# Performance work log

Hardware: AMD Instinct MI355X
Metric: run time of the kernel (lower is better)

Reference implementation:

```python
import jax, jax.numpy as jnp
import numpy as np

FS = 11      # filter_size per spatial dim
N_ITER = 5   # mean-field iterations


def _gaussian_kernel1d(inv_theta, spacing, fs):
    # distances scaled by per-sample spacing; center tap zeroed (message passing excludes self)
    d = spacing * jnp.arange(-(fs // 2), fs // 2 + 1, dtype=jnp.float32)
    k = jnp.exp(-(d * inv_theta) ** 2 / 2)
    return k * (1.0 - jax.nn.one_hot(fs // 2, fs, dtype=k.dtype))


def _conv1d_last(x, kernel):
    # valid cross-correlation along the last axis; kernel is symmetric so conv == corr
    xr = x.reshape(-1, 1, x.shape[-1])
    out = jax.lax.conv_general_dilated(xr, kernel.reshape(1, 1, -1), (1,), 'VALID')
    return out.reshape(*x.shape[:-1], out.shape[-1])


def _smooth_single(x, spacing, inv_theta):
    # x: (C, H, W) -> separable zero-center Gaussian filter, per-sample kernels
    p = FS // 2
    x = jnp.pad(x, ((0, 0), (p, p), (p, p)))
    kh = _gaussian_kernel1d(inv_theta[0], spacing[0], FS)
    kw = _gaussian_kernel1d(inv_theta[1], spacing[1], FS)
    x = _conv1d_last(jnp.swapaxes(x, 1, 2), kh)  # conv along H -> (C, W+2p, H)
    x = _conv1d_last(jnp.swapaxes(x, 1, 2), kw)  # conv along W -> (C, H, W)
    return x


def setup_inputs() -> dict:
    key = jax.random.key(0)
    k1, = jax.random.split(key, 1)
    x = jax.random.normal(k1, (8, 19, 512, 512), dtype=jnp.float32)
    spatial_spacings = jnp.ones((8, 2), dtype=jnp.float32)
    smoothness_weight = jnp.array(1.0, dtype=jnp.float32)
    inv_smoothness_theta = jnp.ones((2,), dtype=jnp.float32)  # 1 / smoothness_theta
    return {"x": x, "spatial_spacings": spatial_spacings,
            "smoothness_weight": smoothness_weight,
            "inv_smoothness_theta": inv_smoothness_theta}


def reference(x, spatial_spacings, smoothness_weight, inv_smoothness_theta):
    n_classes = x.shape[1]
    comp = -jnp.eye(n_classes, dtype=x.dtype)  # compatibility matrix -(l1 == l2)
    negative_unary = x
    smooth = jax.vmap(_smooth_single, in_axes=(0, 0, None))
    for _ in range(N_ITER):
        q = jax.nn.softmax(x, axis=1)
        m = smoothness_weight * smooth(q, spatial_spacings, inv_smoothness_theta)
        m = jnp.einsum('bchw,cd->bdhw', m, comp)
        x = negative_unary - m
    return x  # returns='logits'
```

## Files before the change

### kernel.cpp

```cpp
#include <hip/hip_runtime.h>

#define FS 11
#define HFS 5

constexpr int Bn = 8, Cn = 19, Hn = 512, Wn = 512;
constexpr int HWn = Hn * Wn;
constexpr int CHWn = Cn * HWn;
constexpr int TOTn = Bn * CHWn;

constexpr int TH = 32, TW = 64;
constexpr int HR  = TH + 10;
constexpr int HC4 = 20;
constexpr int NP4 = HR * HC4;
constexpr int QS  = 84;
constexpr int WSS = 68;

__global__ void k_taps(const float* __restrict__ spacing,
                       const float* __restrict__ inv_theta,
                       const float* __restrict__ wgt,
                       float* __restrict__ taps) {
    int t = threadIdx.x;
    if (t < Bn * 2 * FS) {
        int j = t % FS;
        int dim = (t / FS) & 1;
        int b = t / (2 * FS);
        float d = spacing[b * 2 + dim] * (float)(j - HFS);
        float a = d * inv_theta[dim];
        float k = __expf(-0.5f * a * a);
        if (j == HFS) k = 0.0f;
        if (dim == 1) k *= wgt[0];
        taps[t] = k;
    }
}

__global__ __launch_bounds__(256, 4) void k_fused(const float* __restrict__ xin,
                                                  const float* __restrict__ x0,
                                                  float* __restrict__ xout,
                                                  const float* __restrict__ taps) {
    __shared__ float srinv[HR * QS];
    __shared__ float qs[HR * QS];
    __shared__ float ws[HR * WSS];

    const int tid = threadIdx.x;
    const int w0 = blockIdx.x * TW;
    const int h0 = blockIdx.y * TH;
    const int b  = blockIdx.z;

    const float* tp = taps + b * (2 * FS);
    float kh[FS], kw[FS];
#pragma unroll
    for (int j = 0; j < FS; j++) { kh[j] = tp[j]; kw[j] = tp[FS + j]; }

    const float* xb = xin + b * CHWn;

#pragma unroll 1
    for (int k = 0; k < 4; ++k) {
        int i = tid + 256 * k;
        if (i >= NP4) break;
        int r  = i / HC4, c4 = i % HC4;
        int hh = h0 - 5 + r;
        int ww = w0 - 8 + 4 * c4;
        if (hh >= 0 && hh < Hn && ww >= 0 && ww <= Wn - 4) {
            const float* p = xb + hh * Wn + ww;
            float4 s = {0.f, 0.f, 0.f, 0.f};
#pragma unroll
            for (int c = 0; c < Cn; ++c) {
                float4 v = *(const float4*)(p + c * HWn);
                s.x += __expf(v.x); s.y += __expf(v.y);
                s.z += __expf(v.z); s.w += __expf(v.w);
            }
            float4 rv = {1.f / s.x, 1.f / s.y, 1.f / s.z, 1.f / s.w};
            *(float4*)&srinv[r * QS + 4 * c4] = rv;
        }
    }
    __syncthreads();

    for (int c = 0; c < Cn; ++c) {
        const float* xc = xb + c * HWn;

#pragma unroll 1
        for (int k = 0; k < 4; ++k) {
            int i = tid + 256 * k;
            if (i >= NP4) break;
            int r  = i / HC4, c4 = i % HC4;
            int hh = h0 - 5 + r;
            int ww = w0 - 8 + 4 * c4;
            float4 qv = {0.f, 0.f, 0.f, 0.f};
            if (hh >= 0 && hh < Hn && ww >= 0 && ww <= Wn - 4) {
                float4 v  = *(const float4*)(xc + hh * Wn + ww);
                float4 rv = *(const float4*)&srinv[r * QS + 4 * c4];
                qv.x = __expf(v.x) * rv.x; qv.y = __expf(v.y) * rv.y;
                qv.z = __expf(v.z) * rv.z; qv.w = __expf(v.w) * rv.w;
            }
            *(float4*)&qs[r * QS + 4 * c4] = qv;
        }
        __syncthreads();

#pragma unroll 1
        for (int i = tid; i < HR * 8; i += 256) {
            int r = i >> 3, g = i & 7;
            float t[24];
#pragma unroll
            for (int m = 0; m < 6; ++m)
                *(float4*)&t[4 * m] = *(const float4*)&qs[r * QS + 8 * g + 4 * m];
            float o[8];
#pragma unroll
            for (int k2 = 0; k2 < 8; ++k2) {
                float a = 0.f;
#pragma unroll
                for (int j = 0; j < FS; ++j) {
                    if (j == HFS) continue;
                    a = fmaf(kw[j], t[k2 + 3 + j], a);
                }
                o[k2] = a;
            }
            float4 oa = {o[0], o[1], o[2], o[3]};
            float4 ob = {o[4], o[5], o[6], o[7]};
            *(float4*)&ws[r * WSS + 8 * g]     = oa;
            *(float4*)&ws[r * WSS + 8 * g + 4] = ob;
        }
        __syncthreads();

        {
            int rs = tid >> 4, cg = tid & 15;
            int t0 = 2 * rs, col = 4 * cg;
            float4 wv[12];
#pragma unroll
            for (int j = 0; j < 12; ++j)
                wv[j] = *(const float4*)&ws[(t0 + j) * WSS + col];
            float4 o0 = {0.f, 0.f, 0.f, 0.f}, o1 = {0.f, 0.f, 0.f, 0.f};
#pragma unroll
            for (int j = 0; j < FS; ++j) {
                if (j == HFS) continue;
                float kj = kh[j];
                o0.x = fmaf(kj, wv[j].x, o0.x);     o0.y = fmaf(kj, wv[j].y, o0.y);
                o0.z = fmaf(kj, wv[j].z, o0.z);     o0.w = fmaf(kj, wv[j].w, o0.w);
                o1.x = fmaf(kj, wv[j + 1].x, o1.x); o1.y = fmaf(kj, wv[j + 1].y, o1.y);
                o1.z = fmaf(kj, wv[j + 1].z, o1.z); o1.w = fmaf(kj, wv[j + 1].w, o1.w);
            }
            int gi = (b * Cn + c) * HWn + (h0 + t0) * Wn + (w0 + col);
            float4 xa = *(const float4*)(x0 + gi);
            float4 xc2 = *(const float4*)(x0 + gi + Wn);
            float4 ra = {xa.x + o0.x, xa.y + o0.y, xa.z + o0.z, xa.w + o0.w};
            float4 rb = {xc2.x + o1.x, xc2.y + o1.y, xc2.z + o1.z, xc2.w + o1.w};
            *(float4*)(xout + gi)      = ra;
            *(float4*)(xout + gi + Wn) = rb;
        }
    }
}

extern "C" void kernel_launch(void* const* d_in, const int* in_sizes, int n_in,
                              void* d_out, int out_size, void* d_ws, size_t ws_size,
                              hipStream_t stream) {
    const float* x0      = (const float*)d_in[0];
    const float* spacing = (const float*)d_in[1];
    const float* wgt     = (const float*)d_in[2];
    const float* itheta  = (const float*)d_in[3];
    float* out = (float*)d_out;

    float* A    = (float*)d_ws;
    float* taps = A + TOTn;

    k_taps<<<1, 256, 0, stream>>>(spacing, itheta, wgt, taps);

    dim3 g(Wn / TW, Hn / TH, Bn);

    k_fused<<<g, 256, 0, stream>>>(x0,  x0, out, taps);
    k_fused<<<g, 256, 0, stream>>>(out, x0, A,   taps);
    k_fused<<<g, 256, 0, stream>>>(A,   x0, out, taps);
    k_fused<<<g, 256, 0, stream>>>(out, x0, A,   taps);
    k_fused<<<g, 256, 0, stream>>>(A,   x0, out, taps);
}
```

Before: 980.7 us.

## Keep softmax normalizers in registers and prefetch next channel loads

Moves the per-pixel softmax reciprocal sums from shared memory into registers, with each thread handling up to four float4 positions whose offsets are precomputed once. The next channel's halo input and the current channel's residual x0 values are loaded before the horizontal and vertical passes so their global latency overlaps compute. Filter taps are made wave-uniform with readfirstlane. This frees LDS and removes a barrier, at the cost of higher register pressure under the launch bound of 4 blocks.

```diff
diff --git a/kernel.cpp b/kernel.cpp
--- a/kernel.cpp
+++ b/kernel.cpp
@@ -14,6 +14,10 @@
 constexpr int NP4 = HR * HC4;
 constexpr int QS  = 84;
 constexpr int WSS = 68;
+
+__device__ __forceinline__ float rfl(float x) {
+    return __uint_as_float(__builtin_amdgcn_readfirstlane(__float_as_uint(x)));
+}
 
 __global__ void k_taps(const float* __restrict__ spacing,
                        const float* __restrict__ inv_theta,
@@ -37,7 +41,6 @@
                                                   const float* __restrict__ x0,
                                                   float* __restrict__ xout,
                                                   const float* __restrict__ taps) {
-    __shared__ float srinv[HR * QS];
     __shared__ float qs[HR * QS];
     __shared__ float ws[HR * WSS];
 
@@ -49,56 +52,85 @@
     const float* tp = taps + b * (2 * FS);
     float kh[FS], kw[FS];
 #pragma unroll
-    for (int j = 0; j < FS; j++) { kh[j] = tp[j]; kw[j] = tp[FS + j]; }
+    for (int j = 0; j < FS; j++) { kh[j] = rfl(tp[j]); kw[j] = rfl(tp[FS + j]); }
 
     const float* xb = xin + b * CHWn;
 
-#pragma unroll 1
-    for (int k = 0; k < 4; ++k) {
+    int off[4], lo[4];
+    bool act[4], it[4];
+#pragma unroll
+    for (int k = 0; k < 4; k++) {
         int i = tid + 256 * k;
-        if (i >= NP4) break;
-        int r  = i / HC4, c4 = i % HC4;
+        it[k] = (i < NP4);
+        int r = i / HC4, c4 = i % HC4;
         int hh = h0 - 5 + r;
         int ww = w0 - 8 + 4 * c4;
-        if (hh >= 0 && hh < Hn && ww >= 0 && ww <= Wn - 4) {
-            const float* p = xb + hh * Wn + ww;
-            float4 s = {0.f, 0.f, 0.f, 0.f};
-#pragma unroll
-            for (int c = 0; c < Cn; ++c) {
-                float4 v = *(const float4*)(p + c * HWn);
-                s.x += __expf(v.x); s.y += __expf(v.y);
-                s.z += __expf(v.z); s.w += __expf(v.w);
-            }
-            float4 rv = {1.f / s.x, 1.f / s.y, 1.f / s.z, 1.f / s.w};
-            *(float4*)&srinv[r * QS + 4 * c4] = rv;
-        }
-    }
-    __syncthreads();
+        act[k] = it[k] && hh >= 0 && hh < Hn && ww >= 0 && ww <= Wn - 4;
+        off[k] = hh * Wn + ww;
+        lo[k]  = r * QS + 4 * c4;
+    }
+
+    float4 px[4], rinv[4];
+    {
+        float4 s[4];
+#pragma unroll
+        for (int k = 0; k < 4; k++) {
+            s[k] = make_float4(0.f, 0.f, 0.f, 0.f);
+            if (act[k]) {
+                float4 v = *(const float4*)(xb + off[k]);
+                px[k] = v;
+                s[k].x = __expf(v.x); s[k].y = __expf(v.y);
+                s[k].z = __expf(v.z); s[k].w = __expf(v.w);
+            }
+        }
+#pragma unroll 2
+        for (int c = 1; c < Cn; ++c) {
+#pragma unroll
+            for (int k = 0; k < 4; k++) {
+                if (!act[k]) continue;
+                float4 v = *(const float4*)(xb + c * HWn + off[k]);
+                s[k].x += __expf(v.x); s[k].y += __expf(v.y);
+                s[k].z += __expf(v.z); s[k].w += __expf(v.w);
+            }
+        }
+#pragma unroll
+        for (int k = 0; k < 4; k++)
+            if (act[k])
+                rinv[k] = make_float4(1.f / s[k].x, 1.f / s[k].y,
+                                      1.f / s[k].z, 1.f / s[k].w);
+    }
+
+    const int t0  = 2 * (tid >> 4);
+    const int col = 4 * (tid & 15);
+    const int pix = (h0 + t0) * Wn + (w0 + col);
 
     for (int c = 0; c < Cn; ++c) {
-        const float* xc = xb + c * HWn;
+#pragma unroll
+        for (int k = 0; k < 4; k++) {
+            if (!it[k]) continue;
+            float4 qv = make_float4(0.f, 0.f, 0.f, 0.f);
+            if (act[k]) {
+                qv.x = __expf(px[k].x) * rinv[k].x;
+                qv.y = __expf(px[k].y) * rinv[k].y;
+                qv.z = __expf(px[k].z) * rinv[k].z;
+                qv.w = __expf(px[k].w) * rinv[k].w;
+            }
+            *(float4*)&qs[lo[k]] = qv;
+        }
+        __syncthreads();
+
+        if (c + 1 < Cn) {
+#pragma unroll
+            for (int k = 0; k < 4; k++)
+                if (act[k]) px[k] = *(const float4*)(xb + (c + 1) * HWn + off[k]);
+        }
+        const int gi = (b * Cn + c) * HWn + pix;
+        float4 xA = *(const float4*)(x0 + gi);
+        float4 xB = *(const float4*)(x0 + gi + Wn);
 
 #pragma unroll 1
-        for (int k = 0; k < 4; ++k) {
-            int i = tid + 256 * k;
-            if (i >= NP4) break;
-            int r  = i / HC4, c4 = i % HC4;
-            int hh = h0 - 5 + r;
-            int ww = w0 - 8 + 4 * c4;
-            float4 qv = {0.f, 0.f, 0.f, 0.f};
-            if (hh >= 0 && hh < Hn && ww >= 0 && ww <= Wn - 4) {
-                float4 v  = *(const float4*)(xc + hh * Wn + ww);
-                float4 rv = *(const float4*)&srinv[r * QS + 4 * c4];
-                qv.x = __expf(v.x) * rv.x; qv.y = __expf(v.y) * rv.y;
-                qv.z = __expf(v.z) * rv.z; qv.w = __expf(v.w) * rv.w;
-            }
-            *(float4*)&qs[r * QS + 4 * c4] = qv;
-        }
-        __syncthreads();
-
-#pragma unroll 1
-        for (int i = tid; i < HR * 8; i += 256) {
-            int r = i >> 3, g = i & 7;
+        for (int i2 = tid; i2 < HR * 8; i2 += 256) {
+            int r = i2 >> 3, g = i2 & 7;
             float t[24];
 #pragma unroll
             for (int m = 0; m < 6; ++m)
@@ -122,8 +154,6 @@
         __syncthreads();
 
         {
-            int rs = tid >> 4, cg = tid & 15;
-            int t0 = 2 * rs, col = 4 * cg;
             float4 wv[12];
 #pragma unroll
             for (int j = 0; j < 12; ++j)
@@ -138,11 +168,8 @@
                 o1.x = fmaf(kj, wv[j + 1].x, o1.x); o1.y = fmaf(kj, wv[j + 1].y, o1.y);
                 o1.z = fmaf(kj, wv[j + 1].z, o1.z); o1.w = fmaf(kj, wv[j + 1].w, o1.w);
             }
-            int gi = (b * Cn + c) * HWn + (h0 + t0) * Wn + (w0 + col);
-            float4 xa = *(const float4*)(x0 + gi);
-            float4 xc2 = *(const float4*)(x0 + gi + Wn);
-            float4 ra = {xa.x + o0.x, xa.y + o0.y, xa.z + o0.z, xa.w + o0.w};
-            float4 rb = {xc2.x + o1.x, xc2.y + o1.y, xc2.z + o1.z, xc2.w + o1.w};
+            float4 ra = {xA.x + o0.x, xA.y + o0.y, xA.z + o0.z, xA.w + o0.w};
+            float4 rb = {xB.x + o1.x, xB.y + o1.y, xB.z + o1.z, xB.w + o1.w};
             *(float4*)(xout + gi)      = ra;
             *(float4*)(xout + gi + Wn) = rb;
         }
```

After: 899.2 us. 1.09x faster.

## Keep softmax in registers, double-buffer row-pass smem and remap blocks

Applied to the files above, without the earlier changes.

The softmax normalizer and the per-channel exp are now computed in registers by the threads that do the horizontal pass, so the q staging buffer and the srinv buffer in shared memory go away. The horizontal-pass output is double-buffered, which lets the vertical pass for channel c-1 overlap with loading and filtering channel c, using one barrier per channel instead of two. Blocks are remapped through a 1D grid swizzle so that consecutive blocks fall on different batches, and the filter taps are made wave-uniform with readfirstlane. The cost is much higher register pressure from the two 18-element normalizer arrays and the staged loads, which may spill or reduce occupancy.

```diff
diff --git a/kernel.cpp b/kernel.cpp
--- a/kernel.cpp
+++ b/kernel.cpp
@@ -10,10 +10,12 @@
 
 constexpr int TH = 32, TW = 64;
 constexpr int HR  = TH + 10;
-constexpr int HC4 = 20;
-constexpr int NP4 = HR * HC4;
-constexpr int QS  = 84;
+constexpr int NT  = HR * 8;
 constexpr int WSS = 68;
+
+__device__ __forceinline__ float rfl(float x) {
+    return __uint_as_float(__builtin_amdgcn_readfirstlane(__float_as_uint(x)));
+}
 
 __global__ void k_taps(const float* __restrict__ spacing,
                        const float* __restrict__ inv_theta,
@@ -33,120 +35,149 @@
     }
 }
 
+#define PASS1(XO, VM, RI) do {                                                   \
+    float s_[18];                                                                \
+    _Pragma("unroll") for (int i = 0; i < 18; ++i) s_[i] = 0.f;                  \
+    for (int c_ = Cn - 1; c_ >= 0; --c_) {                                       \
+        float4 p_[6];                                                            \
+        _Pragma("unroll") for (int m = 0; m < 6; ++m) {                          \
+            float4 v_ = {0.f, 0.f, 0.f, 0.f};                                    \
+            if (((VM) >> m) & 1) v_ = *(const float4*)(xb + c_ * HWn + (XO) + 4 * m); \
+            p_[m] = v_; }                                                        \
+        const float* pf_ = (const float*)p_;                                     \
+        _Pragma("unroll") for (int i = 0; i < 18; ++i) s_[i] += __expf(pf_[i + 3]); \
+    }                                                                            \
+    _Pragma("unroll") for (int i = 0; i < 18; ++i) RI[i] = 1.f / s_[i];          \
+} while (0)
+
+#define A_STAGE(PX, RI, VM, LO, BUF) do {                                        \
+    const float* pf_ = (const float*)(PX);                                       \
+    float q_[18];                                                                \
+    _Pragma("unroll") for (int i = 0; i < 18; ++i) {                             \
+        float e_ = __expf(pf_[i + 3]) * RI[i];                                   \
+        q_[i] = (((VM) >> ((i + 3) >> 2)) & 1) ? e_ : 0.f; }                     \
+    float o_[8];                                                                 \
+    _Pragma("unroll") for (int k_ = 0; k_ < 8; ++k_) {                           \
+        float a_ = 0.f;                                                          \
+        _Pragma("unroll") for (int j_ = 0; j_ < FS; ++j_) {                      \
+            if (j_ == HFS) continue;                                             \
+            a_ = fmaf(kw[j_], q_[k_ + j_], a_); }                                \
+        o_[k_] = a_; }                                                           \
+    float4 oa_ = {o_[0], o_[1], o_[2], o_[3]};                                   \
+    float4 ob_ = {o_[4], o_[5], o_[6], o_[7]};                                   \
+    *(float4*)&ws[BUF][(LO)]     = oa_;                                          \
+    *(float4*)&ws[BUF][(LO) + 4] = ob_;                                          \
+} while (0)
+
+#define B_PHASE(CC, XA, XB) do {                                                 \
+    const float* wb_ = ws[(CC) & 1];                                             \
+    float4 o0_ = {0.f, 0.f, 0.f, 0.f}, o1_ = {0.f, 0.f, 0.f, 0.f};               \
+    _Pragma("unroll") for (int j_ = 0; j_ < 12; ++j_) {                          \
+        float4 v_ = *(const float4*)&wb_[bws + j_ * WSS];                        \
+        if (j_ < 11 && j_ != HFS) { float kj_ = kh[j_];                          \
+            o0_.x = fmaf(kj_, v_.x, o0_.x); o0_.y = fmaf(kj_, v_.y, o0_.y);      \
+            o0_.z = fmaf(kj_, v_.z, o0_.z); o0_.w = fmaf(kj_, v_.w, o0_.w); }    \
+        if (j_ >= 1 && j_ != HFS + 1) { float kj_ = kh[j_ - 1];                  \
+            o1_.x = fmaf(kj_, v_.x, o1_.x); o1_.y = fmaf(kj_, v_.y, o1_.y);      \
+            o1_.z = fmaf(kj_, v_.z, o1_.z); o1_.w = fmaf(kj_, v_.w, o1_.w); } }  \
+    int gi_ = (b * Cn + (CC)) * HWn + pix;                                       \
+    float4 ra_ = {(XA).x + o0_.x, (XA).y + o0_.y, (XA).z + o0_.z, (XA).w + o0_.w}; \
+    float4 rb_ = {(XB).x + o1_.x, (XB).y + o1_.y, (XB).z + o1_.z, (XB).w + o1_.w}; \
+    *(float4*)(xout + gi_)      = ra_;                                           \
+    *(float4*)(xout + gi_ + Wn) = rb_;                                           \
+} while (0)
+
 __global__ __launch_bounds__(256, 4) void k_fused(const float* __restrict__ xin,
                                                   const float* __restrict__ x0,
                                                   float* __restrict__ xout,
                                                   const float* __restrict__ taps) {
-    __shared__ float srinv[HR * QS];
-    __shared__ float qs[HR * QS];
-    __shared__ float ws[HR * WSS];
+    __shared__ float ws[2][HR * WSS];
 
     const int tid = threadIdx.x;
-    const int w0 = blockIdx.x * TW;
-    const int h0 = blockIdx.y * TH;
-    const int b  = blockIdx.z;
+    const int id = blockIdx.x;
+    const int fl = (id & 7) * 128 + (id >> 3);
+    const int b  = fl >> 7;
+    const int ty = (fl & 127) >> 3, tx = fl & 7;
+    const int h0 = ty * TH, w0 = tx * TW;
 
     const float* tp = taps + b * (2 * FS);
     float kh[FS], kw[FS];
 #pragma unroll
-    for (int j = 0; j < FS; j++) { kh[j] = tp[j]; kw[j] = tp[FS + j]; }
+    for (int j = 0; j < FS; j++) { kh[j] = rfl(tp[j]); kw[j] = rfl(tp[FS + j]); }
 
     const float* xb = xin + b * CHWn;
 
+    int xo1 = 0, lo1 = 0, vm1 = 0, xo2 = 0, lo2 = 0, vm2 = 0;
+    {
+        int r = tid >> 3, g = tid & 7;
+        int hh = h0 - 5 + r, wc = w0 - 8 + 8 * g;
+        xo1 = hh * Wn + wc; lo1 = r * WSS + 8 * g;
+        if (hh >= 0 && hh < Hn) {
+#pragma unroll
+            for (int m = 0; m < 6; ++m)
+                if (wc + 4 * m >= 0 && wc + 4 * m <= Wn - 4) vm1 |= 1 << m;
+        }
+    }
+    const bool dual = tid < (NT - 256);
+    if (dual) {
+        int t2 = tid + 256;
+        int r = t2 >> 3, g = t2 & 7;
+        int hh = h0 - 5 + r, wc = w0 - 8 + 8 * g;
+        xo2 = hh * Wn + wc; lo2 = r * WSS + 8 * g;
+        if (hh >= 0 && hh < Hn) {
+#pragma unroll
+            for (int m = 0; m < 6; ++m)
+                if (wc + 4 * m >= 0 && wc + 4 * m <= Wn - 4) vm2 |= 1 << m;
+        }
+    }
+
+    {
+        float4 z = {0.f, 0.f, 0.f, 0.f};
+        if (!vm1) { *(float4*)&ws[0][lo1] = z; *(float4*)&ws[0][lo1 + 4] = z;
+                    *(float4*)&ws[1][lo1] = z; *(float4*)&ws[1][lo1 + 4] = z; }
+        if (dual && !vm2) { *(float4*)&ws[0][lo2] = z; *(float4*)&ws[0][lo2 + 4] = z;
+                            *(float4*)&ws[1][lo2] = z; *(float4*)&ws[1][lo2 + 4] = z; }
+    }
+
+    float ri1[18], ri2[18];
+    if (vm1) PASS1(xo1, vm1, ri1);
+    if (dual && vm2) PASS1(xo2, vm2, ri2);
+
+    const int rs = tid >> 4, cg = tid & 15;
+    const int bws = 2 * rs * WSS + 4 * cg;
+    const int pix = (h0 + 2 * rs) * Wn + (w0 + 4 * cg);
+
+    float4 xA = {0.f, 0.f, 0.f, 0.f}, xB = xA;
+
 #pragma unroll 1
-    for (int k = 0; k < 4; ++k) {
-        int i = tid + 256 * k;
-        if (i >= NP4) break;
-        int r  = i / HC4, c4 = i % HC4;
-        int hh = h0 - 5 + r;
-        int ww = w0 - 8 + 4 * c4;
-        if (hh >= 0 && hh < Hn && ww >= 0 && ww <= Wn - 4) {
-            const float* p = xb + hh * Wn + ww;
-            float4 s = {0.f, 0.f, 0.f, 0.f};
-#pragma unroll
-            for (int c = 0; c < Cn; ++c) {
-                float4 v = *(const float4*)(p + c * HWn);
-                s.x += __expf(v.x); s.y += __expf(v.y);
-                s.z += __expf(v.z); s.w += __expf(v.w);
+    for (int c = 0; c < Cn; ++c) {
+        float4 p1[6];
+#pragma unroll
+        for (int m = 0; m < 6; ++m) {
+            float4 v = {0.f, 0.f, 0.f, 0.f};
+            if ((vm1 >> m) & 1) v = *(const float4*)(xb + c * HWn + xo1 + 4 * m);
+            p1[m] = v;
+        }
+        if (c > 0) B_PHASE(c - 1, xA, xB);
+        {
+            int gi = (b * Cn + c) * HWn + pix;
+            xA = *(const float4*)(x0 + gi);
+            xB = *(const float4*)(x0 + gi + Wn);
+        }
+        if (vm1) A_STAGE(p1, ri1, vm1, lo1, (c & 1));
+        if (dual && vm2) {
+            float4 p2[6];
+#pragma unroll
+            for (int m = 0; m < 6; ++m) {
+                float4 v = {0.f, 0.f, 0.f, 0.f};
+                if ((vm2 >> m) & 1) v = *(const float4*)(xb + c * HWn + xo2 + 4 * m);
+                p2[m] = v;
             }
-            float4 rv = {1.f / s.x, 1.f / s.y, 1.f / s.z, 1.f / s.w};
-            *(float4*)&srinv[r * QS + 4 * c4] = rv;
-        }
-    }
-    __syncthreads();
-
-    for (int c = 0; c < Cn; ++c) {
-        const float* xc = xb + c * HWn;
-
-#pragma unroll 1
-        for (int k = 0; k < 4; ++k) {
-            int i = tid + 256 * k;
-            if (i >= NP4) break;
-            int r  = i / HC4, c4 = i % HC4;
-            int hh = h0 - 5 + r;
-            int ww = w0 - 8 + 4 * c4;
-            float4 qv = {0.f, 0.f, 0.f, 0.f};
-            if (hh >= 0 && hh < Hn && ww >= 0 && ww <= Wn - 4) {
-                float4 v  = *(const float4*)(xc + hh * Wn + ww);
-                float4 rv = *(const float4*)&srinv[r * QS + 4 * c4];
-                qv.x = __expf(v.x) * rv.x; qv.y = __expf(v.y) * rv.y;
-                qv.z = __expf(v.z) * rv.z; qv.w = __expf(v.w) * rv.w;
-            }
-            *(float4*)&qs[r * QS + 4 * c4] = qv;
+            A_STAGE(p2, ri2, vm2, lo2, (c & 1));
         }
         __syncthreads();
-
-#pragma unroll 1
-        for (int i = tid; i < HR * 8; i += 256) {
-            int r = i >> 3, g = i & 7;
-            float t[24];
-#pragma unroll
-            for (int m = 0; m < 6; ++m)
-                *(float4*)&t[4 * m] = *(const float4*)&qs[r * QS + 8 * g + 4 * m];
-            float o[8];
-#pragma unroll
-            for (int k2 = 0; k2 < 8; ++k2) {
-                float a = 0.f;
-#pragma unroll
-                for (int j = 0; j < FS; ++j) {
-                    if (j == HFS) continue;
-                    a = fmaf(kw[j], t[k2 + 3 + j], a);
-                }
-                o[k2] = a;
-            }
-            float4 oa = {o[0], o[1], o[2], o[3]};
-            float4 ob = {o[4], o[5], o[6], o[7]};
-            *(float4*)&ws[r * WSS + 8 * g]     = oa;
-            *(float4*)&ws[r * WSS + 8 * g + 4] = ob;
-        }
-        __syncthreads();
-
-        {
-            int rs = tid >> 4, cg = tid & 15;
-            int t0 = 2 * rs, col = 4 * cg;
-            float4 wv[12];
-#pragma unroll
-            for (int j = 0; j < 12; ++j)
-                wv[j] = *(const float4*)&ws[(t0 + j) * WSS + col];
-            float4 o0 = {0.f, 0.f, 0.f, 0.f}, o1 = {0.f, 0.f, 0.f, 0.f};
-#pragma unroll
-            for (int j = 0; j < FS; ++j) {
-                if (j == HFS) continue;
-                float kj = kh[j];
-                o0.x = fmaf(kj, wv[j].x, o0.x);     o0.y = fmaf(kj, wv[j].y, o0.y);
-                o0.z = fmaf(kj, wv[j].z, o0.z);     o0.w = fmaf(kj, wv[j].w, o0.w);
-                o1.x = fmaf(kj, wv[j + 1].x, o1.x); o1.y = fmaf(kj, wv[j + 1].y, o1.y);
-                o1.z = fmaf(kj, wv[j + 1].z, o1.z); o1.w = fmaf(kj, wv[j + 1].w, o1.w);
-            }
-            int gi = (b * Cn + c) * HWn + (h0 + t0) * Wn + (w0 + col);
-            float4 xa = *(const float4*)(x0 + gi);
-            float4 xc2 = *(const float4*)(x0 + gi + Wn);
-            float4 ra = {xa.x + o0.x, xa.y + o0.y, xa.z + o0.z, xa.w + o0.w};
-            float4 rb = {xc2.x + o1.x, xc2.y + o1.y, xc2.z + o1.z, xc2.w + o1.w};
-            *(float4*)(xout + gi)      = ra;
-            *(float4*)(xout + gi + Wn) = rb;
-        }
-    }
+    }
+    B_PHASE(Cn - 1, xA, xB);
 }
 
 extern "C" void kernel_launch(void* const* d_in, const int* in_sizes, int n_in,
@@ -163,11 +194,9 @@
 
     k_taps<<<1, 256, 0, stream>>>(spacing, itheta, wgt, taps);
 
-    dim3 g(Wn / TW, Hn / TH, Bn);
-
-    k_fused<<<g, 256, 0, stream>>>(x0,  x0, out, taps);
-    k_fused<<<g, 256, 0, stream>>>(out, x0, A,   taps);
-    k_fused<<<g, 256, 0, stream>>>(A,   x0, out, taps);
-    k_fused<<<g, 256, 0, stream>>>(out, x0, A,   taps);
-    k_fused<<<g, 256, 0, stream>>>(A,   x0, out, taps);
-}
+    k_fused<<<1024, 256, 0, stream>>>(x0,  x0, out, taps);
+    k_fused<<<1024, 256, 0, stream>>>(out, x0, A,   taps);
+    k_fused<<<1024, 256, 0, stream>>>(A,   x0, out, taps);
+    k_fused<<<1024, 256, 0, stream>>>(out, x0, A,   taps);
+    k_fused<<<1024, 256, 0, stream>>>(A,   x0, out, taps);
+}
```

Result: faster. 953.6 us (-2.8%).
